# Performance work log

Hardware: AMD Instinct MI355X
Metric: run time of the kernel (lower is better)

## Reference

```python
import jax, jax.numpy as jnp
import numpy as np

T, H, W, C, HD, K = 4, 128, 128, 256, 8, 9
F = C // HD


def setup_inputs() -> dict:
    key = jax.random.key(0)
    ks = jax.random.split(key, 6)
    x = jax.random.normal(ks[0], (T, H, W, C), jnp.float32)
    attn = jax.random.uniform(ks[1], (1, HD, T, H, W, K), jnp.float32)
    attn = attn / attn.sum(-1, keepdims=True)  # softmax-normalized neighbor weights
    # integer flow offsets (dt, dh, dw) in [-3, 3], as produced by non-local search
    flows = jax.random.randint(ks[2], (1, HD, T, H, W, K, 3), -3, 4, jnp.int32)
    v_w = jax.random.normal(ks[3], (C, C), jnp.float32) * (C ** -0.5)
    proj_w = jax.random.normal(ks[4], (C, C), jnp.float32) * (C ** -0.5)
    proj_b = jnp.zeros((C,), jnp.float32)
    return dict(x=x, attn=attn, flows=flows, v_w=v_w, proj_w=proj_w, proj_b=proj_b)


def reference(x, attn, flows, v_w, proj_w, proj_b):
    T, H, W, C = x.shape
    HD = attn.shape[1]
    F = C // HD
    # v projection, split heads: [T,H,W,HD,F]
    v = (x @ v_w.T).reshape(T, H, W, HD, F)
    fl = flows[0]  # [HD,T,H,W,K,3] integer offsets (dt, dh, dw)
    tt = jnp.clip(jnp.arange(T)[None, :, None, None, None] + fl[..., 0], 0, T - 1)
    hh = jnp.clip(jnp.arange(H)[None, None, :, None, None] + fl[..., 1], 0, H - 1)
    ww = jnp.clip(jnp.arange(W)[None, None, None, :, None] + fl[..., 2], 0, W - 1)
    hd = jnp.arange(HD)[:, None, None, None, None]
    # flow-guided non-local gather: [HD,T,H,W,K,F]
    gathered = v[tt, hh, ww, hd]
    # attention-weighted sum over K neighbors, merge heads: [T,H,W,C]
    out = jnp.einsum('dthwk,dthwkf->thwdf', attn[0], gathered).reshape(T, H, W, C)
    # output projection
    return out @ proj_w.T + proj_b
```

## Files before the change

### kernel.cpp

```cpp
#include <hip/hip_runtime.h>
#include <hip/hip_bf16.h>

namespace {

constexpr int T = 4, H = 128, W = 128, C = 256, HD = 8, K = 9, F = 32;
constexpr int M = T * H * W;

typedef __attribute__((ext_vector_type(8))) short short8v;
typedef __attribute__((ext_vector_type(4))) float f32x4;

__device__ __forceinline__ unsigned short f2bf(float f) {
  unsigned u = __float_as_uint(f);
  unsigned r = (u + 0x7fffu + ((u >> 16) & 1u)) >> 16;
  return (unsigned short)r;
}

__device__ __forceinline__ float bf2f(unsigned short u) {
  return __uint_as_float(((unsigned)u) << 16);
}

template <bool A_BF16, bool OUT_F32>
__global__ __launch_bounds__(256) void mfma_gemm(
    const void* __restrict__ Aptr, const float* __restrict__ Bw,
    void* __restrict__ Cptr, const float* __restrict__ bias) {
  __shared__ unsigned short As[128][40];
  __shared__ unsigned short Bs[128][40];
  const int m0 = blockIdx.x * 128;
  const int n0 = blockIdx.y * 128;
  const int t = threadIdx.x;
  const int lane = t & 63;
  const int wid = t >> 6;
  const int wm = wid >> 1, wn = wid & 1;
  const int fr = lane & 15;
  const int kg = lane >> 4;

  f32x4 acc[4][4];
#pragma unroll
  for (int ni = 0; ni < 4; ++ni) {
    float b = 0.f;
    if (OUT_F32) b = bias[n0 + wn * 64 + ni * 16 + fr];
#pragma unroll
    for (int mi = 0; mi < 4; ++mi) {
      acc[mi][ni][0] = b; acc[mi][ni][1] = b;
      acc[mi][ni][2] = b; acc[mi][ni][3] = b;
    }
  }

  for (int k0 = 0; k0 < C; k0 += 32) {
    __syncthreads();
    if (A_BF16) {
      const unsigned short* Ab = (const unsigned short*)Aptr;
#pragma unroll
      for (int i = 0; i < 2; ++i) {
        const int flat = t + i * 256;
        const int row = flat >> 2, kc = (flat & 3) * 8;
        *(short8v*)&As[row][kc] =
            *(const short8v*)(Ab + (size_t)(m0 + row) * C + k0 + kc);
      }
    } else {
      const float* Af = (const float*)Aptr;
#pragma unroll
      for (int i = 0; i < 4; ++i) {
        const int flat = t + i * 256;
        const int row = flat >> 3, kc = (flat & 7) * 4;
        const float4 v4 = *(const float4*)(Af + (size_t)(m0 + row) * C + k0 + kc);
        ushort4 o;
        o.x = f2bf(v4.x); o.y = f2bf(v4.y); o.z = f2bf(v4.z); o.w = f2bf(v4.w);
        *(ushort4*)&As[row][kc] = o;
      }
    }
#pragma unroll
    for (int i = 0; i < 4; ++i) {
      const int flat = t + i * 256;
      const int row = flat >> 3, kc = (flat & 7) * 4;
      const float4 v4 = *(const float4*)(Bw + (size_t)(n0 + row) * C + k0 + kc);
      ushort4 o;
      o.x = f2bf(v4.x); o.y = f2bf(v4.y); o.z = f2bf(v4.z); o.w = f2bf(v4.w);
      *(ushort4*)&Bs[row][kc] = o;
    }
    __syncthreads();
    short8v af[4], bfv[4];
#pragma unroll
    for (int mi = 0; mi < 4; ++mi)
      af[mi] = *(const short8v*)&As[wm * 64 + mi * 16 + fr][kg * 8];
#pragma unroll
    for (int ni = 0; ni < 4; ++ni)
      bfv[ni] = *(const short8v*)&Bs[wn * 64 + ni * 16 + fr][kg * 8];
#pragma unroll
    for (int mi = 0; mi < 4; ++mi)
#pragma unroll
      for (int ni = 0; ni < 4; ++ni)
        acc[mi][ni] = __builtin_amdgcn_mfma_f32_16x16x32_bf16(
            af[mi], bfv[ni], acc[mi][ni], 0, 0, 0);
  }

#pragma unroll
  for (int mi = 0; mi < 4; ++mi) {
#pragma unroll
    for (int ni = 0; ni < 4; ++ni) {
      const int gcol = n0 + wn * 64 + ni * 16 + fr;
#pragma unroll
      for (int r = 0; r < 4; ++r) {
        const int grow = m0 + wm * 64 + mi * 16 + kg * 4 + r;
        if (OUT_F32) {
          ((float*)Cptr)[(size_t)grow * C + gcol] = acc[mi][ni][r];
        } else {
          ((unsigned short*)Cptr)[(size_t)grow * C + gcol] = f2bf(acc[mi][ni][r]);
        }
      }
    }
  }
}

__global__ __launch_bounds__(256) void gather_kernel(
    const unsigned short* __restrict__ v, const float* __restrict__ attn,
    const int* __restrict__ flows, unsigned short* __restrict__ agg) {
  const int g = blockIdx.x * 256 + threadIdx.x;
  const int pair = g >> 2;
  const int fq = g & 3;
  const int head = pair >> 16;
  const int m = pair & 65535;
  const int t = m >> 14;
  const int h = (m >> 7) & 127;
  const int w = m & 127;
  const int base = pair * K;
  const int fbase = base * 3;
  const int foff = head * F + fq * 8;

  float facc[8] = {0.f, 0.f, 0.f, 0.f, 0.f, 0.f, 0.f, 0.f};
#pragma unroll
  for (int k = 0; k < K; ++k) {
    const int dt = flows[fbase + k * 3 + 0];
    const int dh = flows[fbase + k * 3 + 1];
    const int dw = flows[fbase + k * 3 + 2];
    const float aw = attn[base + k];
    const int tt = min(max(t + dt, 0), T - 1);
    const int hh = min(max(h + dh, 0), H - 1);
    const int ww = min(max(w + dw, 0), W - 1);
    const int mm = (tt << 14) | (hh << 7) | ww;
    const short8v r8 = *(const short8v*)(v + (size_t)mm * C + foff);
#pragma unroll
    for (int j = 0; j < 8; ++j)
      facc[j] += aw * bf2f((unsigned short)r8[j]);
  }
  short8v o;
#pragma unroll
  for (int j = 0; j < 8; ++j) o[j] = (short)f2bf(facc[j]);
  *(short8v*)(agg + (size_t)m * C + foff) = o;
}

__global__ __launch_bounds__(256) void agg_proj_kernel(
    const unsigned short* __restrict__ v, const float* __restrict__ attn,
    const int* __restrict__ flows, const float* __restrict__ proj_w,
    const float* __restrict__ proj_b, float* __restrict__ out) {
  __shared__ float Agg[32][C];
  __shared__ float Bs[32][C];
  const int bid = blockIdx.x;
  const int t = bid >> 9;
  const int h0 = ((bid >> 5) & 15) * 8;
  const int w0 = (bid & 31) * 4;
  const int tid = threadIdx.x;

  const int g = tid >> 3;
  const int f4 = (tid & 7) * 4;
#pragma unroll
  for (int r = 0; r < 8; ++r) {
    const int pi = r * 32 + g;
    const int pos = pi >> 3;
    const int head = pi & 7;
    const int h = h0 + (pos >> 2);
    const int w = w0 + (pos & 3);
    const int base = (((head * T + t) * H + h) * W + w) * K;
    const int fbase = base * 3;
    float4 acc = {0.f, 0.f, 0.f, 0.f};
#pragma unroll
    for (int k = 0; k < K; ++k) {
      const int dt = flows[fbase + k * 3 + 0];
      const int dh = flows[fbase + k * 3 + 1];
      const int dw = flows[fbase + k * 3 + 2];
      const float aw = attn[base + k];
      const int tt = min(max(t + dt, 0), T - 1);
      const int hh = min(max(h + dh, 0), H - 1);
      const int ww = min(max(w + dw, 0), W - 1);
      const int mm = (tt * H + hh) * W + ww;
      const ushort4 r4 = *(const ushort4*)(v + (size_t)mm * C + head * F + f4);
      acc.x += aw * bf2f(r4.x);
      acc.y += aw * bf2f(r4.y);
      acc.z += aw * bf2f(r4.z);
      acc.w += aw * bf2f(r4.w);
    }
    *(float4*)&Agg[pos][head * F + f4] = acc;
  }
  __syncthreads();

  const int tx = tid & 31;
  const int ty = tid >> 5;
  float acc2[4][8];
  {
    const float4 b0 = *(const float4*)(proj_b + tx * 8);
    const float4 b1 = *(const float4*)(proj_b + tx * 8 + 4);
#pragma unroll
    for (int i = 0; i < 4; ++i) {
      acc2[i][0] = b0.x; acc2[i][1] = b0.y; acc2[i][2] = b0.z; acc2[i][3] = b0.w;
      acc2[i][4] = b1.x; acc2[i][5] = b1.y; acc2[i][6] = b1.z; acc2[i][7] = b1.w;
    }
  }
  for (int k0 = 0; k0 < C; k0 += 32) {
#pragma unroll
    for (int i = 0; i < 8; ++i) {
      const float4 w4 = *(const float4*)(proj_w + (size_t)tid * C + k0 + i * 4);
      Bs[i * 4 + 0][tid] = w4.x;
      Bs[i * 4 + 1][tid] = w4.y;
      Bs[i * 4 + 2][tid] = w4.z;
      Bs[i * 4 + 3][tid] = w4.w;
    }
    __syncthreads();
#pragma unroll 4
    for (int kk = 0; kk < 32; ++kk) {
      const float4 bb0 = *(const float4*)&Bs[kk][tx * 8];
      const float4 bb1 = *(const float4*)&Bs[kk][tx * 8 + 4];
      float a[4];
#pragma unroll
      for (int i = 0; i < 4; ++i) a[i] = Agg[ty * 4 + i][k0 + kk];
#pragma unroll
      for (int i = 0; i < 4; ++i) {
        acc2[i][0] += a[i] * bb0.x;
        acc2[i][1] += a[i] * bb0.y;
        acc2[i][2] += a[i] * bb0.z;
        acc2[i][3] += a[i] * bb0.w;
        acc2[i][4] += a[i] * bb1.x;
        acc2[i][5] += a[i] * bb1.y;
        acc2[i][6] += a[i] * bb1.z;
        acc2[i][7] += a[i] * bb1.w;
      }
    }
    __syncthreads();
  }
#pragma unroll
  for (int i = 0; i < 4; ++i) {
    const int pos = ty * 4 + i;
    const int h = h0 + (pos >> 2);
    const int w = w0 + (pos & 3);
    const int m = (t * H + h) * W + w;
    float4 o0, o1;
    o0.x = acc2[i][0]; o0.y = acc2[i][1]; o0.z = acc2[i][2]; o0.w = acc2[i][3];
    o1.x = acc2[i][4]; o1.y = acc2[i][5]; o1.z = acc2[i][6]; o1.w = acc2[i][7];
    *(float4*)(out + (size_t)m * C + tx * 8) = o0;
    *(float4*)(out + (size_t)m * C + tx * 8 + 4) = o1;
  }
}

}

extern "C" void kernel_launch(void* const* d_in, const int* in_sizes, int n_in,
                              void* d_out, int out_size, void* d_ws,
                              size_t ws_size, hipStream_t stream) {
  const float* x = (const float*)d_in[0];
  const float* attn = (const float*)d_in[1];
  const int* flows = (const int*)d_in[2];
  const float* v_w = (const float*)d_in[3];
  const float* proj_w = (const float*)d_in[4];
  const float* proj_b = (const float*)d_in[5];
  float* out = (float*)d_out;

  const size_t VBYTES = (size_t)M * C * 2;
  unsigned short* v = (unsigned short*)d_ws;

  dim3 g1(M / 128, C / 128);
  mfma_gemm<false, false><<<g1, 256, 0, stream>>>(x, v_w, v, nullptr);

  if (ws_size >= 2 * VBYTES) {
    unsigned short* agg = (unsigned short*)((char*)d_ws + VBYTES);
    gather_kernel<<<(M * HD * 4) / 256, 256, 0, stream>>>(v, attn, flows, agg);
    mfma_gemm<true, true><<<g1, 256, 0, stream>>>(agg, proj_w, out, proj_b);
  } else {
    const int nblk = T * (H / 8) * (W / 4);
    agg_proj_kernel<<<nblk, 256, 0, stream>>>(v, attn, flows, proj_w, proj_b,
                                              out);
  }
}
```

Baseline: 114.6 us.

## Restructure gather kernel into spatial 8x8 tiles with all heads per block

The gather kernel now assigns each block an 8x8 spatial tile at one time step. Within a block all 8 heads and 4 feature quarters are covered, and each thread loops over 8 rows. Blocks are launched in an interleaved order so that neighbouring gathers of v share cache lines across heads and stay in L2. Flow and attention loads become nontemporal and are hoisted ahead of the v loads to raise memory-level parallelism. The launch drops to 1024 blocks, which reduces parallelism per wave but spreads work over more iterations per thread.

```diff
diff --git a/kernel.cpp b/kernel.cpp
--- a/kernel.cpp
+++ b/kernel.cpp
@@ -115,38 +115,51 @@
 __global__ __launch_bounds__(256) void gather_kernel(
     const unsigned short* __restrict__ v, const float* __restrict__ attn,
     const int* __restrict__ flows, unsigned short* __restrict__ agg) {
-  const int g = blockIdx.x * 256 + threadIdx.x;
-  const int pair = g >> 2;
-  const int fq = g & 3;
-  const int head = pair >> 16;
-  const int m = pair & 65535;
-  const int t = m >> 14;
-  const int h = (m >> 7) & 127;
-  const int w = m & 127;
-  const int base = pair * K;
-  const int fbase = base * 3;
+  const int bid = (blockIdx.x & 7) * 128 + (blockIdx.x >> 3);
+  const int t = bid & 3;
+  const int w0 = ((bid >> 2) & 15) * 8;
+  const int h0 = (bid >> 6) * 8;
+  const int tid = threadIdx.x;
+  const int fq = tid & 3;
+  const int head = (tid >> 2) & 7;
+  const int pw = tid >> 5;
   const int foff = head * F + fq * 8;
 
-  float facc[8] = {0.f, 0.f, 0.f, 0.f, 0.f, 0.f, 0.f, 0.f};
-#pragma unroll
-  for (int k = 0; k < K; ++k) {
-    const int dt = flows[fbase + k * 3 + 0];
-    const int dh = flows[fbase + k * 3 + 1];
-    const int dw = flows[fbase + k * 3 + 2];
-    const float aw = attn[base + k];
-    const int tt = min(max(t + dt, 0), T - 1);
-    const int hh = min(max(h + dh, 0), H - 1);
-    const int ww = min(max(w + dw, 0), W - 1);
-    const int mm = (tt << 14) | (hh << 7) | ww;
-    const short8v r8 = *(const short8v*)(v + (size_t)mm * C + foff);
-#pragma unroll
-    for (int j = 0; j < 8; ++j)
-      facc[j] += aw * bf2f((unsigned short)r8[j]);
-  }
-  short8v o;
-#pragma unroll
-  for (int j = 0; j < 8; ++j) o[j] = (short)f2bf(facc[j]);
-  *(short8v*)(agg + (size_t)m * C + foff) = o;
+#pragma unroll
+  for (int r = 0; r < 8; ++r) {
+    const int h = h0 + r;
+    const int w = w0 + pw;
+    const int m = (t << 14) | (h << 7) | w;
+    const int pair = (head << 16) | m;
+    const int base = pair * K;
+    const int fbase = base * 3;
+
+    int mm[K];
+    float aw[K];
+#pragma unroll
+    for (int k = 0; k < K; ++k) {
+      const int dt = __builtin_nontemporal_load(flows + fbase + k * 3 + 0);
+      const int dh = __builtin_nontemporal_load(flows + fbase + k * 3 + 1);
+      const int dw = __builtin_nontemporal_load(flows + fbase + k * 3 + 2);
+      aw[k] = __builtin_nontemporal_load(attn + base + k);
+      const int tt = min(max(t + dt, 0), T - 1);
+      const int hh = min(max(h + dh, 0), H - 1);
+      const int ww = min(max(w + dw, 0), W - 1);
+      mm[k] = (tt << 14) | (hh << 7) | ww;
+    }
+    float facc[8] = {0.f, 0.f, 0.f, 0.f, 0.f, 0.f, 0.f, 0.f};
+#pragma unroll
+    for (int k = 0; k < K; ++k) {
+      const short8v r8 = *(const short8v*)(v + (size_t)mm[k] * C + foff);
+#pragma unroll
+      for (int j = 0; j < 8; ++j)
+        facc[j] += aw[k] * bf2f((unsigned short)r8[j]);
+    }
+    short8v o;
+#pragma unroll
+    for (int j = 0; j < 8; ++j) o[j] = (short)f2bf(facc[j]);
+    *(short8v*)(agg + (size_t)m * C + foff) = o;
+  }
 }
 
 __global__ __launch_bounds__(256) void agg_proj_kernel(
@@ -271,7 +284,7 @@
 
   if (ws_size >= 2 * VBYTES) {
     unsigned short* agg = (unsigned short*)((char*)d_ws + VBYTES);
-    gather_kernel<<<(M * HD * 4) / 256, 256, 0, stream>>>(v, attn, flows, agg);
+    gather_kernel<<<1024, 256, 0, stream>>>(v, attn, flows, agg);
     mfma_gemm<true, true><<<g1, 256, 0, stream>>>(agg, proj_w, out, proj_b);
   } else {
     const int nblk = T * (H / 8) * (W / 4);
```

Measured after the change: 136.4 us. +19.0%, slower.
